# Performance work log

Measured on AMD Instinct MI355X. Metric: run time of the kernel, lower is better.

The kernel has to match this reference:

```python
import jax, jax.numpy as jnp
import numpy as np
from jax import lax

B, CIN, COUT, H, W, K, PAD = 8, 64, 64, 256, 256, 3, 1

def setup_inputs() -> dict:
    key = jax.random.key(0)
    k1, k2, k3, k4 = jax.random.split(key, 4)
    x = jax.random.normal(k1, (B, CIN, H, W), dtype=jnp.float32)
    mask = (jax.random.uniform(k2, (B, 1, H, W)) < 0.5).astype(jnp.float32)
    fan_in = CIN * K * K
    bound = 1.0 / np.sqrt(fan_in)
    weight = jax.random.uniform(k3, (COUT, CIN, K, K), minval=-bound, maxval=bound, dtype=jnp.float32)
    bias = jax.random.uniform(k4, (COUT,), minval=-bound, maxval=bound, dtype=jnp.float32)
    return {"x": x, "mask": mask, "weight": weight, "bias": bias}

def _masked_conv(x, mask, weight, bias):
    # Standard conv: the original gathers valid unfold columns, matmuls with the
    # flattened weight + bias, and scatters back; zeros elsewhere. Equivalent to
    # (conv(x) + b) * valid, where valid[b,l] = any(mask patch at l != 0).
    conv = lax.conv_general_dilated(
        x, weight,
        window_strides=(1, 1),
        padding=[(PAD, PAD), (PAD, PAD)],
        dimension_numbers=("NCHW", "OIHW", "NCHW"),
    )
    out = conv + bias[None, :, None, None]
    # any(|mask| != 0) over each KxK window == max-pool of |mask| > 0
    pooled = lax.reduce_window(
        jnp.abs(mask), 0.0, lax.max,
        window_dimensions=(1, 1, K, K),
        window_strides=(1, 1, 1, 1),
        padding=[(0, 0), (0, 0), (PAD, PAD), (PAD, PAD)],
    )
    valid = pooled > 0  # [B,1,H,W], broadcasts over channels
    return jnp.where(valid, out, jnp.zeros((), dtype=out.dtype))

def reference(x, mask, weight, bias):
    return _masked_conv(x, mask, weight, bias)
```

## Files before the change

### kernel.cpp

```cpp
#include <hip/hip_runtime.h>


#define B_    8
#define C_    64
#define H_    256
#define W_    256
#define HW_   (H_ * W_)

typedef __attribute__((ext_vector_type(8))) short bf16x8;
typedef __attribute__((ext_vector_type(4))) float f32x4;

__device__ __forceinline__ unsigned short f2bf(float f) {
    unsigned int u = __float_as_uint(f);
    u = (u + 0x7FFFu + ((u >> 16) & 1u)) >> 16;
    return (unsigned short)u;
}

__global__ __launch_bounds__(256) void wconv(const float* __restrict__ wgt,
                                             unsigned short* __restrict__ wsA)
{
    const int gid  = blockIdx.x * 256 + threadIdx.x;
    const int s    = gid >> 8;
    const int rest = gid & 255;
    const int mf   = rest >> 6;
    const int lane = rest & 63;
    const int tap  = s >> 1;
    const int kblk = s & 1;
    const int kh = tap / 3, kw = tap % 3;
    const int co = mf * 16 + (lane & 15);
    unsigned short v[8];
#pragma unroll
    for (int j = 0; j < 8; ++j) {
        const int ci = kblk * 32 + (lane >> 4) * 8 + j;
        v[j] = f2bf(wgt[((co * C_ + ci) * 3 + kh) * 3 + kw]);
    }
    unsigned short* dst = wsA + (size_t)gid * 8;
    *(uint4*)dst = *(const uint4*)v;
}

#define TROWS 6
#define TCOLS 34
#define NU    (TROWS * TCOLS * 8)
#define NCHUNK 4
#define NTAIL (NU - 3 * 512)
#define BUFSZ (TROWS * TCOLS * 64)
#define TILES 8

__global__ __launch_bounds__(512, 4) void masked_conv_mfma(
    const float* __restrict__ x,
    const float* __restrict__ mask,
    const unsigned short* __restrict__ wsA,
    const float* __restrict__ bias,
    float* __restrict__ out)
{
    __shared__ __align__(16) unsigned short xs[2 * BUFSZ];

    const int tid  = threadIdx.x;
    const int wave = tid >> 6;
    const int lane = tid & 63;
    const int l15  = lane & 15;
    const int lq   = lane >> 4;

    const int w0    = blockIdx.x * 32;
    const int hbase = blockIdx.y * (4 * TILES);
    const int b     = blockIdx.z;

    const float* xb = x + (size_t)b * C_ * HW_;
    const float* mb = mask + (size_t)b * HW_;

    const int hrow = wave & 3;
    const int ch   = wave >> 2;
    const int pcol = w0 + (lane & 31);

    int ldsoff[NCHUNK], eoff[NCHUNK], rowk[NCHUNK], okwk[NCHUNK];
#pragma unroll
    for (int k = 0; k < NCHUNK; ++k) {
        const int u0 = tid + (k << 9);
        const int u  = (u0 < NU) ? u0 : 0;
        const int col = u % TCOLS;
        const int t2  = u / TCOLS;
        const int oct = t2 & 7;
        const int row = t2 >> 3;
        const int gw  = w0 - 1 + col;
        okwk[k] = (gw >= 0) & (gw < W_);
        const int gwc = gw < 0 ? 0 : (gw >= W_ ? W_ - 1 : gw);
        eoff[k] = oct * 8 * HW_ + gwc;
        const int c = row * TCOLS + col;
        ldsoff[k] = (c << 6) + ((oct ^ (c & 7)) << 3);
        rowk[k] = row;
    }

    float va[NCHUNK][8];
    int   okf[NCHUNK];

    auto stage_issue = [&](int t) {
        const int h0 = hbase + 4 * t;
#pragma unroll
        for (int k = 0; k < NCHUNK; ++k) {
            const int gh  = h0 - 1 + rowk[k];
            const int okh = (gh >= 0) & (gh < H_);
            const int ghc = gh < 0 ? 0 : (gh >= H_ ? H_ - 1 : gh);
            okf[k] = okwk[k] & okh;
            const float* px = xb + eoff[k] + (size_t)ghc * W_;
#pragma unroll
            for (int j = 0; j < 8; ++j) va[k][j] = px[(size_t)j * HW_];
        }
    };
    auto stage_write = [&](int bsel) {
        unsigned short* dst = xs + bsel * BUFSZ;
#pragma unroll
        for (int k = 0; k < NCHUNK; ++k) {
            if (k == NCHUNK - 1 && tid >= NTAIL) continue;
            unsigned short v[8];
#pragma unroll
            for (int j = 0; j < 8; ++j)
                v[j] = okf[k] ? f2bf(va[k][j]) : (unsigned short)0;
            *(uint4*)&dst[ldsoff[k]] = *(const uint4*)v;
        }
    };

    const bf16x8* wA = (const bf16x8*)wsA;

    stage_issue(0);
    stage_write(0);
    __syncthreads();

#pragma unroll 1
    for (int t = 0; t < TILES; ++t) {
        const int h = hbase + 4 * t + hrow;

        if (t + 1 < TILES) stage_issue(t + 1);

        float mv[9];
        int okm = 0;
        {
            int i = 0;
#pragma unroll
            for (int dh = -1; dh <= 1; ++dh) {
#pragma unroll
                for (int dw = -1; dw <= 1; ++dw, ++i) {
                    const int hh = h + dh;
                    const int ww = pcol + dw;
                    const int ok = (hh >= 0) & (hh < H_) & (ww >= 0) & (ww < W_);
                    mv[i] = mb[ok ? (hh * W_ + ww) : 0];
                    okm |= ok << i;
                }
            }
        }
        __builtin_amdgcn_sched_barrier(0);

        const unsigned short* xbuf = xs + (t & 1) * BUFSZ;
        f32x4 acc[2][2];
#pragma unroll
        for (int mf = 0; mf < 2; ++mf)
#pragma unroll
            for (int nf = 0; nf < 2; ++nf)
                acc[mf][nf] = (f32x4){0.f, 0.f, 0.f, 0.f};

#pragma unroll 1
        for (int kh = 0; kh < 3; ++kh) {
            const int rowbase = (hrow + kh) * TCOLS;
#pragma unroll
            for (int kw = 0; kw < 3; ++kw) {
#pragma unroll
                for (int kblk = 0; kblk < 2; ++kblk) {
                    const int s = (kh * 3 + kw) * 2 + kblk;
                    bf16x8 a[2];
#pragma unroll
                    for (int mf = 0; mf < 2; ++mf)
                        a[mf] = wA[(s * 4 + ch * 2 + mf) * 64 + lane];
                    bf16x8 bfv[2];
#pragma unroll
                    for (int nf = 0; nf < 2; ++nf) {
                        const int cell2 = rowbase + nf * 16 + l15 + kw;
                        const int g = kblk * 4 + lq;
                        bfv[nf] = *(const bf16x8*)
                            &xbuf[(cell2 << 6) + ((g ^ (cell2 & 7)) << 3)];
                    }
#pragma unroll
                    for (int mf = 0; mf < 2; ++mf)
#pragma unroll
                        for (int nf = 0; nf < 2; ++nf)
                            acc[mf][nf] = __builtin_amdgcn_mfma_f32_16x16x32_bf16(
                                a[mf], bfv[nf], acc[mf][nf], 0, 0, 0);
                }
            }
        }

        int valid = 0;
#pragma unroll
        for (int i = 0; i < 9; ++i)
            valid |= ((okm >> i) & 1) & (mv[i] != 0.0f ? 1 : 0);
        const int vn0 = __builtin_amdgcn_ds_bpermute(l15 << 2, valid);
        const int vn1 = __builtin_amdgcn_ds_bpermute((16 + l15) << 2, valid);

        if (t + 1 < TILES) stage_write((t + 1) & 1);
        __syncthreads();

#pragma unroll
        for (int nf = 0; nf < 2; ++nf) {
            const int cloc = nf * 16 + l15;
            const int vn = nf ? vn1 : vn0;
            float* ob = out + ((size_t)(b * C_) * H_ + h) * W_ + w0 + cloc;
#pragma unroll
            for (int mf = 0; mf < 2; ++mf) {
#pragma unroll
                for (int reg = 0; reg < 4; ++reg) {
                    const int co = ch * 32 + mf * 16 + lq * 4 + reg;
                    const float val = vn ? (acc[mf][nf][reg] + bias[co]) : 0.0f;
                    ob[(size_t)co * HW_] = val;
                }
            }
        }
    }
}

extern "C" void kernel_launch(void* const* d_in, const int* in_sizes, int n_in,
                              void* d_out, int out_size, void* d_ws, size_t ws_size,
                              hipStream_t stream) {
    const float* x    = (const float*)d_in[0];
    const float* mask = (const float*)d_in[1];
    const float* wgt  = (const float*)d_in[2];
    const float* bias = (const float*)d_in[3];
    float* out        = (float*)d_out;
    unsigned short* wsA = (unsigned short*)d_ws;

    wconv<<<18, 256, 0, stream>>>(wgt, wsA);

    dim3 grid(W_ / 32, H_ / (4 * TILES), B_);
    masked_conv_mfma<<<grid, 512, 0, stream>>>(x, mask, wsA, bias, out);
}
```

Baseline: 372.7 us.

## Pre-convert input to swizzled bf16 channels-last and stage tiles via direct LDS loads

Adds a pre-pass kernel that converts x from fp32 NCHW to bf16 channels-last, with each pixel's 64 channels pre-swizzled in 8-channel groups. The main conv kernel then stages each halo tile with global_load_lds 16-byte DMA straight into LDS. This removes the per-thread register staging, fp32-to-bf16 conversion and strided channel gathers from the conv kernel's inner loop, and halves the bytes it reads for x. In exchange it adds an extra full pass over x (read fp32, write bf16) and another kernel launch, and its correctness relies on the async LDS loads being waited on before the barriers.

```diff
diff --git a/kernel.cpp b/kernel.cpp
--- a/kernel.cpp
+++ b/kernel.cpp
@@ -14,6 +14,12 @@
     unsigned int u = __float_as_uint(f);
     u = (u + 0x7FFFu + ((u >> 16) & 1u)) >> 16;
     return (unsigned short)u;
+}
+
+__device__ __forceinline__ void gld_lds16(const void* g, void* l) {
+    __builtin_amdgcn_global_load_lds(
+        (const __attribute__((address_space(1))) void*)g,
+        (__attribute__((address_space(3))) void*)l, 16, 0, 0);
 }
 
 __global__ __launch_bounds__(256) void wconv(const float* __restrict__ wgt,
@@ -38,22 +44,41 @@
     *(uint4*)dst = *(const uint4*)v;
 }
 
+__global__ __launch_bounds__(256) void xconv(const float* __restrict__ x,
+                                             unsigned short* __restrict__ xsw)
+{
+    const int gid = blockIdx.x * 256 + threadIdx.x;
+    const int b   = gid >> 16;
+    const int p   = gid & 65535;
+    const int gw  = p & 255;
+    const float* px = x + (size_t)b * (C_ * HW_) + p;
+    unsigned short* dst = xsw + (size_t)gid * 64;
+    const int key = gw & 7;
+#pragma unroll
+    for (int o = 0; o < 8; ++o) {
+        unsigned short v[8];
+#pragma unroll
+        for (int j = 0; j < 8; ++j)
+            v[j] = f2bf(px[(size_t)(o * 8 + j) * HW_]);
+        *(uint4*)&dst[(o ^ key) << 3] = *(const uint4*)v;
+    }
+}
+
 #define TROWS 6
 #define TCOLS 34
-#define NU    (TROWS * TCOLS * 8)
-#define NCHUNK 4
-#define NTAIL (NU - 3 * 512)
-#define BUFSZ (TROWS * TCOLS * 64)
+#define NCELL (TROWS * TCOLS)
+#define NGRAN (NCELL * 8)
+#define BUFSH (NCELL * 64)
 #define TILES 8
 
 __global__ __launch_bounds__(512, 4) void masked_conv_mfma(
-    const float* __restrict__ x,
+    const unsigned short* __restrict__ xsw,
     const float* __restrict__ mask,
     const unsigned short* __restrict__ wsA,
     const float* __restrict__ bias,
     float* __restrict__ out)
 {
-    __shared__ __align__(16) unsigned short xs[2 * BUFSZ];
+    __shared__ __align__(16) unsigned short xs[2 * BUFSH];
 
     const int tid  = threadIdx.x;
     const int wave = tid >> 6;
@@ -65,71 +90,57 @@
     const int hbase = blockIdx.y * (4 * TILES);
     const int b     = blockIdx.z;
 
-    const float* xb = x + (size_t)b * C_ * HW_;
-    const float* mb = mask + (size_t)b * HW_;
-
     const int hrow = wave & 3;
     const int ch   = wave >> 2;
     const int pcol = w0 + (lane & 31);
-
-    int ldsoff[NCHUNK], eoff[NCHUNK], rowk[NCHUNK], okwk[NCHUNK];
-#pragma unroll
-    for (int k = 0; k < NCHUNK; ++k) {
-        const int u0 = tid + (k << 9);
-        const int u  = (u0 < NU) ? u0 : 0;
-        const int col = u % TCOLS;
-        const int t2  = u / TCOLS;
-        const int oct = t2 & 7;
-        const int row = t2 >> 3;
+    const float* mb = mask + (size_t)b * HW_;
+    const unsigned short* xbb = xsw + (((size_t)b) << 16) * 64;
+
+    int rowr[4], okwr[4], gcolr[4];
+#pragma unroll
+    for (int r = 0; r < 4; ++r) {
+        const int g  = (r << 9) + tid;
+        const int gg = (g < NGRAN) ? g : 0;
+        const int cell = gg >> 3, slot = gg & 7;
+        rowr[r] = cell / TCOLS;
+        const int col = cell % TCOLS;
         const int gw  = w0 - 1 + col;
-        okwk[k] = (gw >= 0) & (gw < W_);
+        okwr[r] = (gw >= 0) & (gw < W_);
         const int gwc = gw < 0 ? 0 : (gw >= W_ ? W_ - 1 : gw);
-        eoff[k] = oct * 8 * HW_ + gwc;
-        const int c = row * TCOLS + col;
-        ldsoff[k] = (c << 6) + ((oct ^ (c & 7)) << 3);
-        rowk[k] = row;
-    }
-
-    float va[NCHUNK][8];
-    int   okf[NCHUNK];
-
-    auto stage_issue = [&](int t) {
-        const int h0 = hbase + 4 * t;
-#pragma unroll
-        for (int k = 0; k < NCHUNK; ++k) {
-            const int gh  = h0 - 1 + rowk[k];
-            const int okh = (gh >= 0) & (gh < H_);
-            const int ghc = gh < 0 ? 0 : (gh >= H_ ? H_ - 1 : gh);
-            okf[k] = okwk[k] & okh;
-            const float* px = xb + eoff[k] + (size_t)ghc * W_;
-#pragma unroll
-            for (int j = 0; j < 8; ++j) va[k][j] = px[(size_t)j * HW_];
+        gcolr[r] = gwc * 64 + slot * 8;
+    }
+
+    auto stage = [&](int bsel, int t) {
+        const int h0 = hbase + (t << 2);
+        unsigned short* bufb = xs + bsel * BUFSH;
+#pragma unroll
+        for (int r = 0; r < 4; ++r) {
+            const int g = (r << 9) + tid;
+            if (g < NGRAN) {
+                const int gh  = h0 - 1 + rowr[r];
+                const int okh = (gh >= 0) & (gh < H_);
+                if (okh & okwr[r]) {
+                    unsigned short* ldsb = bufb + (((r << 9) + (wave << 6)) << 3);
+                    const unsigned short* gsrc = xbb + (size_t)gh * (W_ * 64) + gcolr[r];
+                    gld_lds16(gsrc, ldsb);
+                } else {
+                    *(uint4*)&bufb[g << 3] = (uint4){0, 0, 0, 0};
+                }
+            }
         }
     };
-    auto stage_write = [&](int bsel) {
-        unsigned short* dst = xs + bsel * BUFSZ;
-#pragma unroll
-        for (int k = 0; k < NCHUNK; ++k) {
-            if (k == NCHUNK - 1 && tid >= NTAIL) continue;
-            unsigned short v[8];
-#pragma unroll
-            for (int j = 0; j < 8; ++j)
-                v[j] = okf[k] ? f2bf(va[k][j]) : (unsigned short)0;
-            *(uint4*)&dst[ldsoff[k]] = *(const uint4*)v;
-        }
-    };
 
     const bf16x8* wA = (const bf16x8*)wsA;
 
-    stage_issue(0);
-    stage_write(0);
+    stage(0, 0);
+    asm volatile("s_waitcnt vmcnt(0)" ::: "memory");
     __syncthreads();
 
 #pragma unroll 1
     for (int t = 0; t < TILES; ++t) {
-        const int h = hbase + 4 * t + hrow;
-
-        if (t + 1 < TILES) stage_issue(t + 1);
+        const int h = hbase + (t << 2) + hrow;
+
+        if (t + 1 < TILES) stage((t + 1) & 1, t + 1);
 
         float mv[9];
         int okm = 0;
@@ -149,7 +160,7 @@
         }
         __builtin_amdgcn_sched_barrier(0);
 
-        const unsigned short* xbuf = xs + (t & 1) * BUFSZ;
+        const unsigned short* xbuf = xs + (t & 1) * BUFSH;
         f32x4 acc[2][2];
 #pragma unroll
         for (int mf = 0; mf < 2; ++mf)
@@ -162,6 +173,7 @@
             const int rowbase = (hrow + kh) * TCOLS;
 #pragma unroll
             for (int kw = 0; kw < 3; ++kw) {
+                const int keyb = (l15 + kw + 7) & 7;
 #pragma unroll
                 for (int kblk = 0; kblk < 2; ++kblk) {
                     const int s = (kh * 3 + kw) * 2 + kblk;
@@ -175,7 +187,7 @@
                         const int cell2 = rowbase + nf * 16 + l15 + kw;
                         const int g = kblk * 4 + lq;
                         bfv[nf] = *(const bf16x8*)
-                            &xbuf[(cell2 << 6) + ((g ^ (cell2 & 7)) << 3)];
+                            &xbuf[(cell2 << 6) + ((g ^ keyb) << 3)];
                     }
 #pragma unroll
                     for (int mf = 0; mf < 2; ++mf)
@@ -194,7 +206,6 @@
         const int vn0 = __builtin_amdgcn_ds_bpermute(l15 << 2, valid);
         const int vn1 = __builtin_amdgcn_ds_bpermute((16 + l15) << 2, valid);
 
-        if (t + 1 < TILES) stage_write((t + 1) & 1);
         __syncthreads();
 
 #pragma unroll
@@ -224,9 +235,11 @@
     const float* bias = (const float*)d_in[3];
     float* out        = (float*)d_out;
     unsigned short* wsA = (unsigned short*)d_ws;
+    unsigned short* xsw = (unsigned short*)((char*)d_ws + 73728);
 
     wconv<<<18, 256, 0, stream>>>(wgt, wsA);
+    xconv<<<2048, 256, 0, stream>>>(x, xsw);
 
     dim3 grid(W_ / 32, H_ / (4 * TILES), B_);
-    masked_conv_mfma<<<grid, 512, 0, stream>>>(x, mask, wsA, bias, out);
-}
+    masked_conv_mfma<<<grid, 512, 0, stream>>>(xsw, mask, wsA, bias, out);
+}
```

Result: faster. 343.0 us (-8.0%).
